# Optimization experiments

Measured on AMD Instinct MI355X. Metric: run time of the kernel, lower is better.

## Reference

```python
import jax, jax.numpy as jnp
import numpy as np

B, T, C, H = 2, 2048, 1024, 16
D = C // H
EPS = 1e-5

def _layer_norm(x, w, b):
    mu = jnp.mean(x, axis=-1, keepdims=True)
    var = jnp.var(x, axis=-1, keepdims=True)
    return (x - mu) * jax.lax.rsqrt(var + EPS) * w + b

def setup_inputs() -> dict:
    key = jax.random.key(0)
    ks = jax.random.split(key, 8)
    s = 0.02
    return {
        "x": jax.random.normal(ks[0], (B, T, C), jnp.float32),
        "ln1_w": jnp.ones((C,), jnp.float32),
        "ln1_b": jnp.zeros((C,), jnp.float32),
        "wq": jax.random.normal(ks[1], (C, C), jnp.float32) * s,
        "bq": jnp.zeros((C,), jnp.float32),
        "wk": jax.random.normal(ks[2], (C, C), jnp.float32) * s,
        "bk": jnp.zeros((C,), jnp.float32),
        "wv": jax.random.normal(ks[3], (C, C), jnp.float32) * s,
        "bv": jnp.zeros((C,), jnp.float32),
        "wo": jax.random.normal(ks[4], (C, C), jnp.float32) * s,
        "bo": jnp.zeros((C,), jnp.float32),
        "ln2_w": jnp.ones((C,), jnp.float32),
        "ln2_b": jnp.zeros((C,), jnp.float32),
        "w1": jax.random.normal(ks[5], (C, 4 * C), jnp.float32) * s,
        "b1": jnp.zeros((4 * C,), jnp.float32),
        "w2": jax.random.normal(ks[6], (4 * C, C), jnp.float32) * s,
        "b2": jnp.zeros((C,), jnp.float32),
    }

def reference(x, ln1_w, ln1_b, wq, bq, wk, bk, wv, bv, wo, bo,
              ln2_w, ln2_b, w1, b1, w2, b2):
    # --- attention branch ---
    h = _layer_norm(x, ln1_w, ln1_b)
    q = (h @ wq + bq).reshape(B, T, H, D).transpose(0, 2, 1, 3)  # [B,H,T,D]
    k = (h @ wk + bk).reshape(B, T, H, D).transpose(0, 2, 1, 3)
    v = (h @ wv + bv).reshape(B, T, H, D).transpose(0, 2, 1, 3)
    att = jnp.einsum("bhqd,bhkd->bhqk", q, k) * (1.0 / np.sqrt(D))
    causal = jnp.tril(jnp.ones((T, T), dtype=bool))
    att = jnp.where(causal[None, None], att, jnp.float32(-jnp.inf))
    att = jax.nn.softmax(att, axis=-1)
    y = jnp.einsum("bhqk,bhkd->bhqd", att, v)
    y = y.transpose(0, 2, 1, 3).reshape(B, T, C)
    y = y @ wo + bo
    x = x + y
    # --- MLP branch ---
    h = _layer_norm(x, ln2_w, ln2_b)
    h = jax.nn.gelu(h @ w1 + b1, approximate=False)
    h = h @ w2 + b2
    return x + h
```

## Files before the change

kernel.cpp:

```cpp
#include <hip/hip_runtime.h>
#include <hip/hip_bf16.h>
#include <math.h>

#define B_  2
#define T_  2048
#define C_  1024
#define H_  16
#define D_  64
#define BT_ (B_*T_)

typedef __hip_bfloat16 bf16;
typedef short bf16x8 __attribute__((ext_vector_type(8)));
typedef float floatx4 __attribute__((ext_vector_type(4)));

struct alignas(8) bf4 { bf16 v[4]; };

#define GLOAD_LDS16(g, l) __builtin_amdgcn_global_load_lds(            \
    (const __attribute__((address_space(1))) void*)(g),                \
    (__attribute__((address_space(3))) void*)(l), 16, 0, 0)

__global__ __launch_bounds__(256) void ln_bf16_kernel(const float* __restrict__ x,
    const float* __restrict__ w, const float* __restrict__ b,
    bf16* __restrict__ out)
{
    __shared__ float ps[4], ps2[4];
    __shared__ float sm, srs;
    const int row = blockIdx.x;
    const int tid = threadIdx.x;
    float4 v = ((const float4*)(x + (size_t)row * C_))[tid];
    float s  = v.x + v.y + v.z + v.w;
    float s2 = v.x*v.x + v.y*v.y + v.z*v.z + v.w*v.w;
    for (int off = 32; off > 0; off >>= 1) {
        s  += __shfl_down(s,  off);
        s2 += __shfl_down(s2, off);
    }
    const int wid = tid >> 6;
    if ((tid & 63) == 0) { ps[wid] = s; ps2[wid] = s2; }
    __syncthreads();
    if (tid == 0) {
        float ts  = ps[0] + ps[1] + ps[2] + ps[3];
        float ts2 = ps2[0] + ps2[1] + ps2[2] + ps2[3];
        float mean = ts * (1.0f / C_);
        float var  = ts2 * (1.0f / C_) - mean * mean;
        sm  = mean;
        srs = rsqrtf(var + 1e-5f);
    }
    __syncthreads();
    const float mean = sm, rs = srs;
    float4 wv = ((const float4*)w)[tid];
    float4 bv = ((const float4*)b)[tid];
    bf4 o;
    o.v[0] = __float2bfloat16((v.x - mean) * rs * wv.x + bv.x);
    o.v[1] = __float2bfloat16((v.y - mean) * rs * wv.y + bv.y);
    o.v[2] = __float2bfloat16((v.z - mean) * rs * wv.z + bv.z);
    o.v[3] = __float2bfloat16((v.w - mean) * rs * wv.w + bv.w);
    *(bf4*)(out + (size_t)row * C_ + tid * 4) = o;
}

__device__ __forceinline__ void wconv_body(const float* __restrict__ W,
    bf16* __restrict__ Wt, int K, int N, int k0, int n0)
{
    __shared__ float L[64][65];
    const int t = threadIdx.x;
    const int r = t >> 4, c4 = t & 15;
    #pragma unroll
    for (int p = 0; p < 4; ++p) {
        const int kr = p * 16 + r;
        const float4 v = *(const float4*)(W + (size_t)(k0 + kr) * N + n0 + c4 * 4);
        L[kr][c4*4+0] = v.x; L[kr][c4*4+1] = v.y;
        L[kr][c4*4+2] = v.z; L[kr][c4*4+3] = v.w;
    }
    __syncthreads();
    #pragma unroll
    for (int p = 0; p < 4; ++p) {
        const int nr = p * 16 + r;
        bf4 o;
        o.v[0] = __float2bfloat16(L[c4*4+0][nr]);
        o.v[1] = __float2bfloat16(L[c4*4+1][nr]);
        o.v[2] = __float2bfloat16(L[c4*4+2][nr]);
        o.v[3] = __float2bfloat16(L[c4*4+3][nr]);
        *(bf4*)(Wt + (size_t)(n0 + nr) * K + k0 + c4 * 4) = o;
    }
}

__global__ __launch_bounds__(256) void wconv_t_kernel(const float* __restrict__ W,
    bf16* __restrict__ Wt, int K, int N)
{
    wconv_body(W, Wt, K, N, blockIdx.x * 64, blockIdx.y * 64);
}

__global__ __launch_bounds__(256) void wconv4_kernel(
    const float* __restrict__ wq, const float* __restrict__ wk,
    const float* __restrict__ wv, const float* __restrict__ wo,
    bf16* __restrict__ wqkvT, bf16* __restrict__ woT)
{
    const int z = blockIdx.z;
    const float* W = (z == 0) ? wq : (z == 1) ? wk : (z == 2) ? wv : wo;
    bf16* Wt = (z == 3) ? woT : wqkvT + (size_t)z * 1024 * 1024;
    wconv_body(W, Wt, 1024, 1024, blockIdx.x * 64, blockIdx.y * 64);
}

__global__ void bcat_kernel(const float* __restrict__ bq, const float* __restrict__ bk,
                            const float* __restrict__ bv, float* __restrict__ o)
{
    const int i = blockIdx.x * 256 + threadIdx.x;
    float v = (i < 1024) ? bq[i] : (i < 2048 ? bk[i - 1024] : bv[i - 2048]);
    o[i] = v;
}

__global__ __launch_bounds__(256) void splitk_reduce_kernel(
    float* __restrict__ out, const float* __restrict__ p1,
    const float* __restrict__ bias, const float* __restrict__ res)
{
    const size_t i = (size_t)blockIdx.x * 256 + threadIdx.x;
    float4 o = ((const float4*)out)[i];
    const float4 p = ((const float4*)p1)[i];
    const float4 bb = ((const float4*)bias)[i & (C_ / 4 - 1)];
    const float4 xx = ((const float4*)res)[i];
    o.x += p.x + bb.x + xx.x;
    o.y += p.y + bb.y + xx.y;
    o.z += p.z + bb.z + xx.z;
    o.w += p.w + bb.w + xx.w;
    ((float4*)out)[i] = o;
}

template<int TM, int TN>
__global__ __launch_bounds__(256) void mfma_gemm_t(
    const bf16* __restrict__ A, const bf16* __restrict__ Wt,
    const float* __restrict__ bias, const float* __restrict__ res,
    void* __restrict__ outv, bf16* __restrict__ vT, float* __restrict__ psplit,
    int M, int N, int K, int ldk, int mode)
{
    constexpr int MI = TM / 32;
    constexpr int NJ = TN / 32;
    constexpr int NSLOT = (TM + TN) / 64;
    __shared__ __align__(16) bf16 As[TM * 32];
    __shared__ __align__(16) bf16 Bs[TN * 32];
    const int tid = threadIdx.x;
    const int w = tid >> 6, l = tid & 63;
    const int fm = l & 15, qd = l >> 4;
    const int m0 = blockIdx.x * TM, n0 = blockIdx.y * TN;
    const int bz = blockIdx.z;
    const int wr = (w >> 1) * (TM / 2), wc = (w & 1) * (TN / 2);

    const bf16* Ab = A  + (size_t)bz * K;
    const bf16* Wb = Wt + (size_t)bz * K;

    const bf16* gsrc[NSLOT];
    bf16* ldst[NSLOT];
    #pragma unroll
    for (int p = 0; p < NSLOT; ++p) {
        const int s = tid + p * 256;
        if (s < TM * 4) {
            const int row = s >> 2, ch = (s & 3) ^ ((row >> 1) & 3);
            gsrc[p] = Ab + (size_t)(m0 + row) * ldk + ch * 8;
            ldst[p] = As + s * 8;
        } else {
            const int s2 = s - TM * 4;
            const int row = s2 >> 2, ch = (s2 & 3) ^ ((row >> 1) & 3);
            gsrc[p] = Wb + (size_t)(n0 + row) * ldk + ch * 8;
            ldst[p] = Bs + s2 * 8;
        }
    }

    floatx4 acc[MI][NJ] = {};
    const int sw = (qd ^ ((fm >> 1) & 3)) * 8;

    const int nk = K >> 5;
    for (int kk = 0; kk < nk; ++kk) {
        const size_t ko = (size_t)kk * 32;
        __syncthreads();
        #pragma unroll
        for (int p = 0; p < NSLOT; ++p)
            GLOAD_LDS16(gsrc[p] + ko, ldst[p]);
        __syncthreads();
        bf16x8 af[MI], bfr[NJ];
        #pragma unroll
        for (int i = 0; i < MI; ++i)
            af[i] = *(const bf16x8*)(As + (wr + i * 16 + fm) * 32 + sw);
        #pragma unroll
        for (int j = 0; j < NJ; ++j)
            bfr[j] = *(const bf16x8*)(Bs + (wc + j * 16 + fm) * 32 + sw);
        #pragma unroll
        for (int i = 0; i < MI; ++i)
            #pragma unroll
            for (int j = 0; j < NJ; ++j)
                acc[i][j] = __builtin_amdgcn_mfma_f32_16x16x32_bf16(
                    af[i], bfr[j], acc[i][j], 0, 0, 0);
    }

    const int col0 = n0 + wc;
    const int row0 = m0 + wr;
    const bool isv = (mode == 3) && (col0 >= 2048);
    float* po = (mode == 4) ? (bz ? psplit : (float*)outv) : nullptr;
    #pragma unroll
    for (int j = 0; j < NJ; ++j) {
        const int col = col0 + j * 16 + fm;
        const float bb = bias[col];
        const bool isq = (mode == 3) && (col0 + j * 16 < 1024);
        #pragma unroll
        for (int i = 0; i < MI; ++i) {
            const int row = row0 + i * 16 + qd * 4;
            floatx4 a = acc[i][j];
            if (mode == 4) {
                #pragma unroll
                for (int r = 0; r < 4; ++r)
                    po[(size_t)(row + r) * N + col] = a[r];
            } else if (mode == 2) {
                float* o = (float*)outv;
                #pragma unroll
                for (int r = 0; r < 4; ++r)
                    o[(size_t)(row + r) * N + col] =
                        a[r] + bb + res[(size_t)(row + r) * N + col];
            } else if (isv) {
                bf4 pv;
                #pragma unroll
                for (int r = 0; r < 4; ++r) pv.v[r] = __float2bfloat16(a[r] + bb);
                *(bf4*)(vT + (size_t)(col - 2048) * M + row) = pv;
            } else {
                bf16* o = (bf16*)outv;
                #pragma unroll
                for (int r = 0; r < 4; ++r) {
                    float vv = a[r] + bb;
                    if (mode == 1) vv = 0.5f * vv * (1.0f + erff(vv * 0.70710678118f));
                    if (isq) vv *= 0.125f;
                    o[(size_t)(row + r) * N + col] = __float2bfloat16(vv);
                }
            }
        }
    }
}

__global__ __launch_bounds__(256) void attn_mfma_kernel(
    const bf16* __restrict__ qkv, const bf16* __restrict__ vT,
    bf16* __restrict__ y)
{
    const int pi = blockIdx.x, h = blockIdx.y, b = blockIdx.z;
    const int tid = threadIdx.x, w = tid >> 6, l = tid & 63;
    const int fm = l & 15, qd = l >> 4;
    const int qta = pi, qtb = 31 - pi;
    const float M0 = 3.0f;

    __shared__ __align__(16) bf16 Ks[4096];
    __shared__ __align__(16) bf16 Vs[4096];
    __shared__ __align__(16) bf16 Ps[8][1152];

    const int r0 = tid >> 2,         c0 = (tid & 3) ^ ((r0 >> 1) & 3);
    const int r1 = (tid + 256) >> 2, c1 = ((tid + 256) & 3) ^ ((r1 >> 1) & 3);
    const bf16* kbase = qkv + (size_t)(b * T_) * 3072 + 1024 + h * 64;
    const bf16* vbase = vT + (size_t)(h * 64) * BT_ + b * T_;
    const bf16* kg0 = kbase + (size_t)(r0 & 63) * 3072 + (r0 >> 6) * 32 + c0 * 8;
    const bf16* kg1 = kbase + (size_t)(r1 & 63) * 3072 + (r1 >> 6) * 32 + c1 * 8;
    const bf16* vg0 = vbase + (size_t)(r0 & 63) * BT_ + (r0 >> 6) * 32 + c0 * 8;
    const bf16* vg1 = vbase + (size_t)(r1 & 63) * BT_ + (r1 >> 6) * 32 + c1 * 8;
    bf16* ksl0 = Ks + (size_t)(w * 64) * 8;
    bf16* ksl1 = Ks + (size_t)(w * 64 + 256) * 8;
    bf16* vsl0 = Vs + (size_t)(w * 64) * 8;
    bf16* vsl1 = Vs + (size_t)(w * 64 + 256) * 8;

    const bf16* qpa = qkv + (size_t)(b * T_ + qta * 64 + w * 16 + fm) * 3072 + h * 64 + qd * 8;
    const bf16* qpb = qkv + (size_t)(b * T_ + qtb * 64 + w * 16 + fm) * 3072 + h * 64 + qd * 8;
    const bf16x8 qa0 = *(const bf16x8*)qpa, qa1 = *(const bf16x8*)(qpa + 32);
    const bf16x8 qb0 = *(const bf16x8*)qpb, qb1 = *(const bf16x8*)(qpb + 32);

    const int qba = qta * 64 + w * 16 + qd * 4;
    const int qbb = qtb * 64 + w * 16 + qd * 4;
    const int sw = (qd ^ ((fm >> 1) & 3)) * 8;

    float la[4] = {}, lb[4] = {};
    floatx4 Oa[4] = {}, Ob[4] = {};
    bf16* psa = &Ps[w * 2][0];
    bf16* psb = &Ps[w * 2 + 1][0];

    auto tile = [&](const bf16x8 q0, const bf16x8 q1, float* lsum,
                    floatx4* O, bf16* ps, const int kt, const int qt, const int qb) {
        floatx4 S[4];
        #pragma unroll
        for (int nt = 0; nt < 4; ++nt) {
            const int rr = nt * 16 + fm;
            const bf16x8 k0 = *(const bf16x8*)(Ks + rr * 32 + sw);
            const bf16x8 k1 = *(const bf16x8*)(Ks + (64 + rr) * 32 + sw);
            floatx4 s = {};
            s = __builtin_amdgcn_mfma_f32_16x16x32_bf16(q0, k0, s, 0, 0, 0);
            s = __builtin_amdgcn_mfma_f32_16x16x32_bf16(q1, k1, s, 0, 0, 0);
            S[nt] = s;
        }
        if (kt == qt) {
            #pragma unroll
            for (int nt = 0; nt < 4; ++nt) {
                const int key = kt * 64 + nt * 16 + fm;
                #pragma unroll
                for (int r = 0; r < 4; ++r)
                    if (key > qb + r) S[nt][r] = -1e30f;
            }
        }
        #pragma unroll
        for (int nt = 0; nt < 4; ++nt)
            #pragma unroll
            for (int r = 0; r < 4; ++r) {
                const float p = __expf(S[nt][r] - M0);
                lsum[r] += p;
                ps[(qd * 4 + r) * 72 + nt * 16 + fm] = __float2bfloat16(p);
            }
        #pragma unroll
        for (int s2 = 0; s2 < 2; ++s2) {
            const bf16x8 pf = *(const bf16x8*)(ps + fm * 72 + s2 * 32 + qd * 8);
            #pragma unroll
            for (int nt = 0; nt < 4; ++nt) {
                const bf16x8 vf =
                    *(const bf16x8*)(Vs + (s2 * 64 + nt * 16 + fm) * 32 + sw);
                O[nt] = __builtin_amdgcn_mfma_f32_16x16x32_bf16(pf, vf, O[nt], 0, 0, 0);
            }
        }
    };

    for (int kt = 0; kt <= qtb; ++kt) {
        const size_t kOff = (size_t)kt * 64 * 3072;
        const size_t vOff = (size_t)kt * 64;
        __syncthreads();
        GLOAD_LDS16(kg0 + kOff, ksl0);
        GLOAD_LDS16(kg1 + kOff, ksl1);
        GLOAD_LDS16(vg0 + vOff, vsl0);
        GLOAD_LDS16(vg1 + vOff, vsl1);
        __syncthreads();
        tile(qb0, qb1, lb, Ob, psb, kt, qtb, qbb);
        if (kt <= qta)
            tile(qa0, qa1, la, Oa, psa, kt, qta, qba);
    }

    #pragma unroll
    for (int mk = 1; mk < 16; mk <<= 1)
        #pragma unroll
        for (int r = 0; r < 4; ++r) {
            la[r] += __shfl_xor(la[r], mk);
            lb[r] += __shfl_xor(lb[r], mk);
        }

    #pragma unroll
    for (int r = 0; r < 4; ++r) {
        const float inva = 1.0f / la[r];
        const float invb = 1.0f / lb[r];
        const size_t rowa = (size_t)(b * T_) + qba + r;
        const size_t rowb = (size_t)(b * T_) + qbb + r;
        #pragma unroll
        for (int nt = 0; nt < 4; ++nt) {
            y[rowa * C_ + h * 64 + nt * 16 + fm] = __float2bfloat16(Oa[nt][r] * inva);
            y[rowb * C_ + h * 64 + nt * 16 + fm] = __float2bfloat16(Ob[nt][r] * invb);
        }
    }
}

extern "C" void kernel_launch(void* const* d_in, const int* in_sizes, int n_in,
                              void* d_out, int out_size, void* d_ws, size_t ws_size,
                              hipStream_t stream)
{
    const float* x     = (const float*)d_in[0];
    const float* ln1_w = (const float*)d_in[1];
    const float* ln1_b = (const float*)d_in[2];
    const float* wq    = (const float*)d_in[3];
    const float* bq    = (const float*)d_in[4];
    const float* wk    = (const float*)d_in[5];
    const float* bk    = (const float*)d_in[6];
    const float* wv    = (const float*)d_in[7];
    const float* bv    = (const float*)d_in[8];
    const float* wo    = (const float*)d_in[9];
    const float* bo    = (const float*)d_in[10];
    const float* ln2_w = (const float*)d_in[11];
    const float* ln2_b = (const float*)d_in[12];
    const float* w1    = (const float*)d_in[13];
    const float* b1    = (const float*)d_in[14];
    const float* w2    = (const float*)d_in[15];
    const float* b2    = (const float*)d_in[16];
    float* out = (float*)d_out;

    char* ws = (char*)d_ws;
    const size_t MB = 1024 * 1024;
    bf16*  wqkvT = (bf16*)(ws);
    bf16*  woT   = (bf16*)(ws + 6 * MB);
    bf16*  w1T   = (bf16*)(ws + 8 * MB);
    bf16*  w2T   = (bf16*)(ws + 16 * MB);
    float* bqkv  = (float*)(ws + 24 * MB);
    bf16*  h     = (bf16*)(ws + 24 * MB + 65536);
    bf16*  qkv   = (bf16*)(ws + 32 * MB + 65536);
    bf16*  vT    = (bf16*)(ws + 56 * MB + 65536);
    bf16*  y     = (bf16*)(ws + 64 * MB + 65536);
    float* x2    = (float*)(ws + 72 * MB + 65536);
    bf16*  u     = qkv;
    float* p1    = (float*)ws;

    wconv4_kernel<<<dim3(16, 16, 4), 256, 0, stream>>>(wq, wk, wv, wo, wqkvT, woT);
    wconv_t_kernel<<<dim3(16, 64), 256, 0, stream>>>(w1, w1T, 1024, 4096);
    wconv_t_kernel<<<dim3(64, 16), 256, 0, stream>>>(w2, w2T, 4096, 1024);
    bcat_kernel<<<12, 256, 0, stream>>>(bq, bk, bv, bqkv);

    ln_bf16_kernel<<<BT_, 256, 0, stream>>>(x, ln1_w, ln1_b, h);
    mfma_gemm_t<128, 128><<<dim3(32, 24), 256, 0, stream>>>(
        h, wqkvT, bqkv, nullptr, qkv, vT, nullptr, BT_, 3072, C_, C_, 3);
    attn_mfma_kernel<<<dim3(16, H_, B_), 256, 0, stream>>>(qkv, vT, y);
    mfma_gemm_t<128, 64><<<dim3(32, 16), 256, 0, stream>>>(
        y, woT, bo, x, x2, nullptr, nullptr, BT_, C_, C_, C_, 2);

    ln_bf16_kernel<<<BT_, 256, 0, stream>>>(x2, ln2_w, ln2_b, h);
    mfma_gemm_t<128, 128><<<dim3(32, 32), 256, 0, stream>>>(
        h, w1T, b1, nullptr, u, nullptr, nullptr, BT_, 4 * C_, C_, C_, 1);
    mfma_gemm_t<128, 128><<<dim3(32, 8, 2), 256, 0, stream>>>(
        u, w2T, b2, nullptr, out, nullptr, p1, BT_, C_, 2 * C_, 4 * C_, 4);
    splitk_reduce_kernel<<<BT_ * C_ / 1024, 256, 0, stream>>>(out, p1, b2, x2);
}
```

Measured before the change: 398.5 us.

## Use 4-way split-K for MLP down-projection with bf16 partials; merge weight conversions

The second MLP GEMM now splits K four ways instead of two, launching 1024 blocks rather than 512 to fill more compute units. Three of the four partial sums are stored as bf16 to cut partial-buffer traffic, and the reduce kernel sums them with bias and residual. The w1 and w2 weight-conversion launches are merged into one kernel. The trade-offs are reduced precision in the partial sums, extra reduce reads, and reuse of the y buffer as scratch for one partial.

```diff
diff --git a/kernel.cpp b/kernel.cpp
--- a/kernel.cpp
+++ b/kernel.cpp
@@ -83,12 +83,6 @@
     }
 }
 
-__global__ __launch_bounds__(256) void wconv_t_kernel(const float* __restrict__ W,
-    bf16* __restrict__ Wt, int K, int N)
-{
-    wconv_body(W, Wt, K, N, blockIdx.x * 64, blockIdx.y * 64);
-}
-
 __global__ __launch_bounds__(256) void wconv4_kernel(
     const float* __restrict__ wq, const float* __restrict__ wk,
     const float* __restrict__ wv, const float* __restrict__ wo,
@@ -100,6 +94,16 @@
     wconv_body(W, Wt, 1024, 1024, blockIdx.x * 64, blockIdx.y * 64);
 }
 
+__global__ __launch_bounds__(256) void wconv2_kernel(
+    const float* __restrict__ w1, const float* __restrict__ w2,
+    bf16* __restrict__ w1T, bf16* __restrict__ w2T)
+{
+    if (blockIdx.z == 0)
+        wconv_body(w1, w1T, 1024, 4096, blockIdx.x * 64, blockIdx.y * 64);
+    else
+        wconv_body(w2, w2T, 4096, 1024, blockIdx.y * 64, blockIdx.x * 64);
+}
+
 __global__ void bcat_kernel(const float* __restrict__ bq, const float* __restrict__ bk,
                             const float* __restrict__ bv, float* __restrict__ o)
 {
@@ -109,18 +113,35 @@
 }
 
 __global__ __launch_bounds__(256) void splitk_reduce_kernel(
-    float* __restrict__ out, const float* __restrict__ p1,
+    float* __restrict__ out, const bf16* __restrict__ p01,
+    const bf16* __restrict__ p2,
     const float* __restrict__ bias, const float* __restrict__ res)
 {
     const size_t i = (size_t)blockIdx.x * 256 + threadIdx.x;
+    const size_t PS = (size_t)BT_ * C_ / 4;
     float4 o = ((const float4*)out)[i];
-    const float4 p = ((const float4*)p1)[i];
     const float4 bb = ((const float4*)bias)[i & (C_ / 4 - 1)];
     const float4 xx = ((const float4*)res)[i];
-    o.x += p.x + bb.x + xx.x;
-    o.y += p.y + bb.y + xx.y;
-    o.z += p.z + bb.z + xx.z;
-    o.w += p.w + bb.w + xx.w;
+    float a0 = 0, a1 = 0, a2 = 0, a3 = 0;
+    #pragma unroll
+    for (int z = 0; z < 2; ++z) {
+        const bf4 pv = ((const bf4*)p01)[z * PS + i];
+        a0 += __bfloat162float(pv.v[0]);
+        a1 += __bfloat162float(pv.v[1]);
+        a2 += __bfloat162float(pv.v[2]);
+        a3 += __bfloat162float(pv.v[3]);
+    }
+    {
+        const bf4 pv = ((const bf4*)p2)[i];
+        a0 += __bfloat162float(pv.v[0]);
+        a1 += __bfloat162float(pv.v[1]);
+        a2 += __bfloat162float(pv.v[2]);
+        a3 += __bfloat162float(pv.v[3]);
+    }
+    o.x += a0 + bb.x + xx.x;
+    o.y += a1 + bb.y + xx.y;
+    o.z += a2 + bb.z + xx.z;
+    o.w += a3 + bb.w + xx.w;
     ((float4*)out)[i] = o;
 }
 
@@ -128,7 +149,7 @@
 __global__ __launch_bounds__(256) void mfma_gemm_t(
     const bf16* __restrict__ A, const bf16* __restrict__ Wt,
     const float* __restrict__ bias, const float* __restrict__ res,
-    void* __restrict__ outv, bf16* __restrict__ vT, float* __restrict__ psplit,
+    void* __restrict__ outv, bf16* __restrict__ vT, bf16* __restrict__ psplit,
     int M, int N, int K, int ldk, int mode)
 {
     constexpr int MI = TM / 32;
@@ -192,7 +213,6 @@
     const int col0 = n0 + wc;
     const int row0 = m0 + wr;
     const bool isv = (mode == 3) && (col0 >= 2048);
-    float* po = (mode == 4) ? (bz ? psplit : (float*)outv) : nullptr;
     #pragma unroll
     for (int j = 0; j < NJ; ++j) {
         const int col = col0 + j * 16 + fm;
@@ -203,9 +223,17 @@
             const int row = row0 + i * 16 + qd * 4;
             floatx4 a = acc[i][j];
             if (mode == 4) {
-                #pragma unroll
-                for (int r = 0; r < 4; ++r)
-                    po[(size_t)(row + r) * N + col] = a[r];
+                if (bz == 0) {
+                    float* o = (float*)outv;
+                    #pragma unroll
+                    for (int r = 0; r < 4; ++r)
+                        o[(size_t)(row + r) * N + col] = a[r];
+                } else {
+                    bf16* o = (bz < 3) ? psplit + (size_t)(bz - 1) * M * N : vT;
+                    #pragma unroll
+                    for (int r = 0; r < 4; ++r)
+                        o[(size_t)(row + r) * N + col] = __float2bfloat16(a[r]);
+                }
             } else if (mode == 2) {
                 float* o = (float*)outv;
                 #pragma unroll
@@ -386,11 +414,11 @@
     bf16*  y     = (bf16*)(ws + 64 * MB + 65536);
     float* x2    = (float*)(ws + 72 * MB + 65536);
     bf16*  u     = qkv;
-    float* p1    = (float*)ws;
+    bf16*  pk01  = (bf16*)ws;
+    bf16*  pk2   = y;
 
     wconv4_kernel<<<dim3(16, 16, 4), 256, 0, stream>>>(wq, wk, wv, wo, wqkvT, woT);
-    wconv_t_kernel<<<dim3(16, 64), 256, 0, stream>>>(w1, w1T, 1024, 4096);
-    wconv_t_kernel<<<dim3(64, 16), 256, 0, stream>>>(w2, w2T, 4096, 1024);
+    wconv2_kernel<<<dim3(16, 64, 2), 256, 0, stream>>>(w1, w2, w1T, w2T);
     bcat_kernel<<<12, 256, 0, stream>>>(bq, bk, bv, bqkv);
 
     ln_bf16_kernel<<<BT_, 256, 0, stream>>>(x, ln1_w, ln1_b, h);
@@ -403,7 +431,7 @@
     ln_bf16_kernel<<<BT_, 256, 0, stream>>>(x2, ln2_w, ln2_b, h);
     mfma_gemm_t<128, 128><<<dim3(32, 32), 256, 0, stream>>>(
         h, w1T, b1, nullptr, u, nullptr, nullptr, BT_, 4 * C_, C_, C_, 1);
-    mfma_gemm_t<128, 128><<<dim3(32, 8, 2), 256, 0, stream>>>(
-        u, w2T, b2, nullptr, out, nullptr, p1, BT_, C_, 2 * C_, 4 * C_, 4);
-    splitk_reduce_kernel<<<BT_ * C_ / 1024, 256, 0, stream>>>(out, p1, b2, x2);
-}
+    mfma_gemm_t<128, 128><<<dim3(32, 8, 4), 256, 0, stream>>>(
+        u, w2T, b2, nullptr, out, pk2, pk01, BT_, C_, C_, 4 * C_, 4);
+    splitk_reduce_kernel<<<BT_ * C_ / 1024, 256, 0, stream>>>(out, pk01, pk2, b2, x2);
+}
```

Result: slower. 409.1 us (+2.6%).
